# Kernel optimization log

Hardware: AMD Instinct MI355X
Metric: run time of the kernel (lower is better)

The kernel has to match this reference:

```python
import jax, jax.numpy as jnp
import numpy as np
from jax import lax

EPS = 1e-5
DN = ('NCHW', 'OIHW', 'NCHW')


def fastsign(x):
    # forward: sign(x); (STE backward handled in fwdbwd module)
    return jnp.sign(x)


def batchnorm(x, gamma, beta, mean, var):
    # inference-mode BatchNorm2d over channel dim
    inv = gamma / jnp.sqrt(var + EPS)
    return x * inv[None, :, None, None] + (beta - mean * inv)[None, :, None, None]


def avgpool2x2(x):
    B, C, H, W = x.shape
    return x.reshape(B, C, H // 2, 2, W // 2, 2).mean(axis=(3, 5))


def setup_inputs() -> dict:
    key = jax.random.key(0)
    ks = jax.random.split(key, 8)
    inp, B, H, W = 256, 32, 56, 56
    x = jax.random.normal(ks[0], (B, inp, H, W), dtype=jnp.float32)
    w3 = jax.random.normal(ks[1], (inp, inp, 3, 3), dtype=jnp.float32) * 0.05
    g3 = jax.random.uniform(ks[2], (inp,), dtype=jnp.float32, minval=0.5, maxval=1.5)
    b3 = jax.random.normal(ks[3], (inp,), dtype=jnp.float32) * 0.1
    m3 = jax.random.normal(ks[4], (inp,), dtype=jnp.float32) * 0.1
    v3 = jax.random.uniform(ks[5], (inp,), dtype=jnp.float32, minval=0.5, maxval=1.5)
    w1 = jax.random.normal(ks[6], (2 * inp, inp, 1, 1), dtype=jnp.float32) * 0.05
    k2 = jax.random.split(ks[7], 4)
    g1 = jax.random.uniform(k2[0], (2 * inp,), dtype=jnp.float32, minval=0.5, maxval=1.5)
    b1 = jax.random.normal(k2[1], (2 * inp,), dtype=jnp.float32) * 0.1
    m1 = jax.random.normal(k2[2], (2 * inp,), dtype=jnp.float32) * 0.1
    v1 = jax.random.uniform(k2[3], (2 * inp,), dtype=jnp.float32, minval=0.5, maxval=1.5)
    return {"x": x, "w3": w3, "g3": g3, "b3": b3, "m3": m3, "v3": v3,
            "w1": w1, "g1": g1, "b1": b1, "m1": m1, "v1": v1}


def reference(x, w3, g3, b3, m3, v3, w1, g1, b1, m1, v1):
    stride = 2
    # --- conv3x3 branch: binarize act + binarize weight, stride-2 3x3 conv, BN ---
    y = lax.conv_general_dilated(fastsign(x), fastsign(w3),
                                 window_strides=(stride, stride),
                                 padding=((1, 1), (1, 1)),
                                 dimension_numbers=DN)
    y = batchnorm(y, g3, b3, m3, v3)
    # shortcut1: AvgPool2d(2,2) when stride==2
    h = y + avgpool2x2(x)
    # --- pointwise branch: 1x1 binary conv doubling channels, BN ---
    z = lax.conv_general_dilated(fastsign(h), fastsign(w1),
                                 window_strides=(1, 1),
                                 padding=((0, 0), (0, 0)),
                                 dimension_numbers=DN)
    z = batchnorm(z, g1, b1, m1, v1)
    # shortcut2: duplicate channels
    return z + jnp.concatenate((h, h), axis=1)
```

## Files before the change

kernel.cpp:

```cpp
#include <hip/hip_runtime.h>
#include <stdint.h>

#define BB   32
#define CC1  256
#define HH   56
#define WW   56
#define PH   57
#define OHH  28
#define OWW  28
#define NPIX (OHH*OWW)
#define CC2  512
#define EPSV 1e-5f

static __device__ __forceinline__ int popc64(uint64_t v) {
    return __builtin_popcountll(v);
}

__global__ __launch_bounds__(256) void k_binx(const float* __restrict__ x,
                                              uint64_t* __restrict__ xbp,
                                              uint64_t* __restrict__ hbits) {
    int gid = blockIdx.x * 256 + threadIdx.x;
    if (gid < 7296) {
        int b = gid / 228, r = gid % 228;
        xbp[((size_t)(b * PH) * PH + (r >> 2)) * 4 + (r & 3)] = 0ull;
    } else if (gid < 14464) {
        int i = gid - 7296;
        int b = i / 224, r = i % 224;
        xbp[((size_t)(b * PH + (r >> 2) + 1) * PH) * 4 + (r & 3)] = 0ull;
    } else if (gid < 114816) {
        hbits[gid - 14464] = 0ull;
    }

    const int NP = BB * HH * WW;
    int pix = gid % NP;
    int cg  = gid / NP;
    int w = pix % WW;
    int h = (pix / WW) % HH;
    int b = pix / (HH * WW);
    const float* xp = x + ((size_t)(b * CC1 + cg * 64)) * (HH * WW) + h * WW + w;
    uint64_t bits = 0;
    #pragma unroll 8
    for (int c = 0; c < 64; ++c) {
        bits |= (uint64_t)(xp[(size_t)c * (HH * WW)] >= 0.0f) << c;
    }
    xbp[((size_t)((b * PH + h + 1) * PH) + w + 1) * 4 + cg] = bits;
}

__global__ __launch_bounds__(256) void k_packw3(const float* __restrict__ w3,
                                                uint64_t* __restrict__ w3t) {
    int id = blockIdx.x * 256 + threadIdx.x;
    int k   = id % 4;
    int tap = (id / 4) % 9;
    int oc  = id / 36;
    const float* wp = w3 + (size_t)oc * 2304 + (size_t)(k * 64) * 9 + tap;
    uint64_t bits = 0;
    #pragma unroll 8
    for (int c = 0; c < 64; ++c) {
        bits |= (uint64_t)(wp[c * 9] >= 0.0f) << c;
    }
    w3t[((size_t)tap * CC1 + oc) * 4 + k] = bits;
}

__global__ __launch_bounds__(256) void k_prep2(const float* __restrict__ w1,
                                               uint64_t* __restrict__ w1b,
                                               const uint64_t* __restrict__ w3t,
                                               const float* __restrict__ g3,
                                               const float* __restrict__ b3,
                                               const float* __restrict__ m3,
                                               const float* __restrict__ v3,
                                               const float* __restrict__ g1,
                                               const float* __restrict__ b1,
                                               const float* __restrict__ m1,
                                               const float* __restrict__ v1,
                                               float* __restrict__ sc3,
                                               float* __restrict__ bi3,
                                               float* __restrict__ sc1,
                                               float* __restrict__ bi1,
                                               int* __restrict__ ctop,
                                               int* __restrict__ cleft,
                                               int* __restrict__ ccorn) {
    int id = blockIdx.x * 256 + threadIdx.x;
    int k  = id % 4;
    int oc = id / 4;
    const float* wp = w1 + (size_t)oc * 256 + k * 64;
    uint64_t bits = 0;
    #pragma unroll 8
    for (int c = 0; c < 64; ++c) {
        bits |= (uint64_t)(wp[c] >= 0.0f) << c;
    }
    w1b[(size_t)oc * 4 + k] = bits;
    if (k == 0) {
        float s1 = g1[oc] / sqrtf(v1[oc] + EPSV);
        sc1[oc] = s1;
        bi1[oc] = b1[oc] - m1[oc] * s1;
        if (oc < CC1) {
            float s3 = g3[oc] / sqrtf(v3[oc] + EPSV);
            sc3[oc] = s3;
            bi3[oc] = b3[oc] - m3[oc] * s3;
        }
    }
    if (id < CC1) {
        int pt[9];
        #pragma unroll
        for (int t = 0; t < 9; ++t) {
            const uint64_t* p = w3t + ((size_t)t * CC1 + id) * 4;
            pt[t] = popc64(p[0]) + popc64(p[1]) + popc64(p[2]) + popc64(p[3]);
        }
        ctop[id]  = (256 - 2 * pt[0]) + (256 - 2 * pt[1]) + (256 - 2 * pt[2]);
        cleft[id] = (256 - 2 * pt[0]) + (256 - 2 * pt[3]) + (256 - 2 * pt[6]);
        ccorn[id] = (256 - 2 * pt[0]);
    }
}

__global__ __launch_bounds__(256, 4) void k_conv3(const float* __restrict__ x,
                                                  const uint64_t* __restrict__ xbp,
                                                  const uint64_t* __restrict__ w3t,
                                                  const float* __restrict__ sc3,
                                                  const float* __restrict__ bi3,
                                                  const int* __restrict__ ctop,
                                                  const int* __restrict__ cleft,
                                                  const int* __restrict__ ccorn,
                                                  float* __restrict__ hbuf,
                                                  uint64_t* __restrict__ hbits) {
    int loc = blockIdx.x * 256 + threadIdx.x;
    int ow = loc % OWW;
    int oh = (loc / OWW) % OHH;
    int b  = loc / NPIX;
    int ocg = blockIdx.y;

    int tot[8] = {0, 0, 0, 0, 0, 0, 0, 0};
    for (int kh = 0; kh < 3; ++kh) {
        const uint64_t* rp = xbp + ((size_t)((b * PH + 2 * oh + kh) * PH) + 2 * ow) * 4;
        uint64_t t0[4], t1[4], t2[4];
        #pragma unroll
        for (int k = 0; k < 4; ++k) { t0[k] = rp[k]; t1[k] = rp[4 + k]; t2[k] = rp[8 + k]; }
        const uint64_t* wrow = w3t + ((size_t)(kh * 3) * CC1 + ocg * 8) * 4;
        #pragma unroll
        for (int o = 0; o < 8; ++o) {
            const uint64_t* w0  = wrow + (size_t)o * 4;
            const uint64_t* w1p = w0 + (size_t)CC1 * 4;
            const uint64_t* w2p = w0 + (size_t)CC1 * 8;
            int s = tot[o];
            #pragma unroll
            for (int k = 0; k < 4; ++k) s += popc64(t0[k] ^ w0[k]);
            #pragma unroll
            for (int k = 0; k < 4; ++k) s += popc64(t1[k] ^ w1p[k]);
            #pragma unroll
            for (int k = 0; k < 4; ++k) s += popc64(t2[k] ^ w2p[k]);
            tot[o] = s;
        }
    }

    bool top  = (oh == 0);
    bool left = (ow == 0);
    uint64_t hb = 0;
    #pragma unroll
    for (int o = 0; o < 8; ++o) {
        int oc = ocg * 8 + o;
        int corr = (top ? ctop[oc] : 0) + (left ? cleft[oc] : 0)
                 - ((top && left) ? ccorn[oc] : 0);
        float y = (float)(2304 - 2 * tot[o] - corr);
        const float* px = x + ((size_t)(b * CC1 + oc)) * (HH * WW) + (2 * oh) * WW + 2 * ow;
        float2 r0 = *(const float2*)(px);
        float2 r1 = *(const float2*)(px + WW);
        float pool = 0.25f * (r0.x + r0.y + r1.x + r1.y);
        float hv = y * sc3[oc] + bi3[oc] + pool;
        hbuf[((size_t)(b * CC1 + oc)) * NPIX + oh * OWW + ow] = hv;
        hb |= (uint64_t)(hv >= 0.0f) << ((ocg & 7) * 8 + o);
    }
    atomicOr((unsigned long long*)&hbits[(size_t)loc * 4 + (ocg >> 3)],
             (unsigned long long)hb);
}

__global__ __launch_bounds__(256, 4) void k_conv1(const uint64_t* __restrict__ hbits,
                                                  const uint64_t* __restrict__ w1b,
                                                  const float* __restrict__ hbuf,
                                                  const float* __restrict__ sc1,
                                                  const float* __restrict__ bi1,
                                                  float* __restrict__ out) {
    int loc = blockIdx.x * 256 + threadIdx.x;
    int p = loc % NPIX;
    int b = loc / NPIX;
    int ocg = blockIdx.y;

    uint64_t hw[4];
    const uint64_t* hp = hbits + (size_t)loc * 4;
    #pragma unroll
    for (int k = 0; k < 4; ++k) hw[k] = hp[k];

    #pragma unroll
    for (int o = 0; o < 8; ++o) {
        int oc  = ocg * 8 + o;
        int oc2 = oc + CC1;
        const uint64_t* wa = w1b + (size_t)oc  * 4;
        const uint64_t* wb = w1b + (size_t)oc2 * 4;
        int pa = 0, pb = 0;
        #pragma unroll
        for (int k = 0; k < 4; ++k) pa += popc64(hw[k] ^ wa[k]);
        #pragma unroll
        for (int k = 0; k < 4; ++k) pb += popc64(hw[k] ^ wb[k]);
        float hc = hbuf[((size_t)(b * CC1 + oc)) * NPIX + p];
        float za = (float)(256 - 2 * pa) * sc1[oc]  + bi1[oc]  + hc;
        float zb = (float)(256 - 2 * pb) * sc1[oc2] + bi1[oc2] + hc;
        out[((size_t)(b * CC2 + oc))  * NPIX + p] = za;
        out[((size_t)(b * CC2 + oc2)) * NPIX + p] = zb;
    }
}

extern "C" void kernel_launch(void* const* d_in, const int* in_sizes, int n_in,
                              void* d_out, int out_size, void* d_ws, size_t ws_size,
                              hipStream_t stream) {
    const float* x  = (const float*)d_in[0];
    const float* w3 = (const float*)d_in[1];
    const float* g3 = (const float*)d_in[2];
    const float* b3 = (const float*)d_in[3];
    const float* m3 = (const float*)d_in[4];
    const float* v3 = (const float*)d_in[5];
    const float* w1 = (const float*)d_in[6];
    const float* g1 = (const float*)d_in[7];
    const float* b1 = (const float*)d_in[8];
    const float* m1 = (const float*)d_in[9];
    const float* v1 = (const float*)d_in[10];
    float* out = (float*)d_out;

    uint8_t* ws = (uint8_t*)d_ws;
    size_t off = 0;
    uint64_t* xbp   = (uint64_t*)(ws + off); off += (size_t)BB * PH * PH * 4 * 8;
    uint64_t* hbits = (uint64_t*)(ws + off); off += (size_t)BB * NPIX * 4 * 8;
    uint64_t* w3t   = (uint64_t*)(ws + off); off += (size_t)9 * CC1 * 4 * 8;
    uint64_t* w1b   = (uint64_t*)(ws + off); off += (size_t)CC2 * 4 * 8;
    float* sc3 = (float*)(ws + off); off += CC1 * 4;
    float* bi3 = (float*)(ws + off); off += CC1 * 4;
    float* sc1 = (float*)(ws + off); off += CC2 * 4;
    float* bi1 = (float*)(ws + off); off += CC2 * 4;
    int* ctop  = (int*)(ws + off); off += CC1 * 4;
    int* cleft = (int*)(ws + off); off += CC1 * 4;
    int* ccorn = (int*)(ws + off); off += CC1 * 4;
    float* hbuf = (float*)(ws + off);

    k_binx  <<<dim3(401408 / 256), 256, 0, stream>>>(x, xbp, hbits);
    k_packw3<<<dim3(9216 / 256),   256, 0, stream>>>(w3, w3t);
    k_prep2 <<<dim3(2048 / 256),   256, 0, stream>>>(w1, w1b, w3t, g3, b3, m3, v3,
                                                     g1, b1, m1, v1, sc3, bi3, sc1, bi1,
                                                     ctop, cleft, ccorn);
    k_conv3 <<<dim3(98, 32), 256, 0, stream>>>(x, xbp, w3t, sc3, bi3, ctop, cleft, ccorn,
                                               hbuf, hbits);
    k_conv1 <<<dim3(98, 32), 256, 0, stream>>>(hbits, w1b, hbuf, sc1, bi1, out);
}
```

Before: 87.32 us.

## Fuse avgpool into binarize pass and store pool/h intermediates as bf16

The binarize kernel now processes each 2x2 input window per thread. It emits the four sign bit-words and a bf16 pooled average, stored channel-grouped in blocks of 8. The conv3 kernel then reads one 16-byte pooled vector per thread instead of re-reading x from global memory for the shortcut, and writes h as bf16. The conv1 kernel reads that bf16 h. This removes a second full pass over x and halves intermediate traffic, at the cost of bf16 rounding error in the residual terms and possible sign flips of h near zero.

After: 90.09 us. 1.03x slower.

```diff
diff --git a/kernel.cpp b/kernel.cpp
--- a/kernel.cpp
+++ b/kernel.cpp
@@ -12,14 +12,26 @@
 #define CC2  512
 #define EPSV 1e-5f
 
+typedef unsigned short ushortx8 __attribute__((ext_vector_type(8)));
+
 static __device__ __forceinline__ int popc64(uint64_t v) {
     return __builtin_popcountll(v);
 }
-
-__global__ __launch_bounds__(256) void k_binx(const float* __restrict__ x,
-                                              uint64_t* __restrict__ xbp,
-                                              uint64_t* __restrict__ hbits) {
+static __device__ __forceinline__ unsigned short f2bf(float f) {
+    uint32_t u = __float_as_uint(f);
+    u += 0x7FFFu + ((u >> 16) & 1u);
+    return (unsigned short)(u >> 16);
+}
+static __device__ __forceinline__ float bf2f(unsigned short u) {
+    return __uint_as_float(((uint32_t)u) << 16);
+}
+
+__global__ __launch_bounds__(256) void k_binpool(const float* __restrict__ x,
+                                                 uint64_t* __restrict__ xbp,
+                                                 uint64_t* __restrict__ hbits,
+                                                 unsigned short* __restrict__ pool) {
     int gid = blockIdx.x * 256 + threadIdx.x;
+    hbits[gid] = 0ull;
     if (gid < 7296) {
         int b = gid / 228, r = gid % 228;
         xbp[((size_t)(b * PH) * PH + (r >> 2)) * 4 + (r & 3)] = 0ull;
@@ -27,23 +39,39 @@
         int i = gid - 7296;
         int b = i / 224, r = i % 224;
         xbp[((size_t)(b * PH + (r >> 2) + 1) * PH) * 4 + (r & 3)] = 0ull;
-    } else if (gid < 114816) {
-        hbits[gid - 14464] = 0ull;
-    }
-
-    const int NP = BB * HH * WW;
-    int pix = gid % NP;
-    int cg  = gid / NP;
-    int w = pix % WW;
-    int h = (pix / WW) % HH;
-    int b = pix / (HH * WW);
-    const float* xp = x + ((size_t)(b * CC1 + cg * 64)) * (HH * WW) + h * WW + w;
-    uint64_t bits = 0;
-    #pragma unroll 8
-    for (int c = 0; c < 64; ++c) {
-        bits |= (uint64_t)(xp[(size_t)c * (HH * WW)] >= 0.0f) << c;
-    }
-    xbp[((size_t)((b * PH + h + 1) * PH) + w + 1) * 4 + cg] = bits;
+    }
+
+    int cell = gid % NPIX;
+    int cg   = (gid / NPIX) & 3;
+    int b    = gid / (NPIX * 4);
+    int pw = cell % OWW;
+    int ph = cell / OWW;
+    int h0 = 2 * ph, w0 = 2 * pw;
+    const float* base = x + ((size_t)(b * CC1 + cg * 64)) * (HH * WW) + h0 * WW + w0;
+
+    uint64_t s00 = 0, s01 = 0, s10 = 0, s11 = 0;
+    for (int j = 0; j < 8; ++j) {
+        ushortx8 pv;
+        #pragma unroll
+        for (int i = 0; i < 8; ++i) {
+            int c = j * 8 + i;
+            const float* cp = base + (size_t)c * (HH * WW);
+            float2 a = *(const float2*)(cp);
+            float2 d = *(const float2*)(cp + WW);
+            s00 |= (uint64_t)(a.x >= 0.0f) << c;
+            s01 |= (uint64_t)(a.y >= 0.0f) << c;
+            s10 |= (uint64_t)(d.x >= 0.0f) << c;
+            s11 |= (uint64_t)(d.y >= 0.0f) << c;
+            pv[i] = f2bf(0.25f * (a.x + a.y + d.x + d.y));
+        }
+        *(ushortx8*)(pool + ((size_t)((b * 32 + cg * 8 + j) * NPIX + cell)) * 8) = pv;
+    }
+
+    size_t rb = ((size_t)(b * PH + h0 + 1) * PH + w0 + 1) * 4 + cg;
+    xbp[rb]          = s00;
+    xbp[rb + 4]      = s01;
+    xbp[rb + PH * 4]     = s10;
+    xbp[rb + PH * 4 + 4] = s11;
 }
 
 __global__ __launch_bounds__(256) void k_packw3(const float* __restrict__ w3,
@@ -112,19 +140,20 @@
     }
 }
 
-__global__ __launch_bounds__(256, 4) void k_conv3(const float* __restrict__ x,
-                                                  const uint64_t* __restrict__ xbp,
+__global__ __launch_bounds__(256, 4) void k_conv3(const uint64_t* __restrict__ xbp,
                                                   const uint64_t* __restrict__ w3t,
                                                   const float* __restrict__ sc3,
                                                   const float* __restrict__ bi3,
                                                   const int* __restrict__ ctop,
                                                   const int* __restrict__ cleft,
                                                   const int* __restrict__ ccorn,
-                                                  float* __restrict__ hbuf,
+                                                  const unsigned short* __restrict__ pool,
+                                                  unsigned short* __restrict__ hbuf,
                                                   uint64_t* __restrict__ hbits) {
     int loc = blockIdx.x * 256 + threadIdx.x;
-    int ow = loc % OWW;
-    int oh = (loc / OWW) % OHH;
+    int p  = loc % NPIX;
+    int ow = p % OWW;
+    int oh = p / OWW;
     int b  = loc / NPIX;
     int ocg = blockIdx.y;
 
@@ -151,6 +180,8 @@
         }
     }
 
+    ushortx8 pv = *(const ushortx8*)(pool + ((size_t)((b * 32 + ocg) * NPIX + p)) * 8);
+
     bool top  = (oh == 0);
     bool left = (ow == 0);
     uint64_t hb = 0;
@@ -160,12 +191,8 @@
         int corr = (top ? ctop[oc] : 0) + (left ? cleft[oc] : 0)
                  - ((top && left) ? ccorn[oc] : 0);
         float y = (float)(2304 - 2 * tot[o] - corr);
-        const float* px = x + ((size_t)(b * CC1 + oc)) * (HH * WW) + (2 * oh) * WW + 2 * ow;
-        float2 r0 = *(const float2*)(px);
-        float2 r1 = *(const float2*)(px + WW);
-        float pool = 0.25f * (r0.x + r0.y + r1.x + r1.y);
-        float hv = y * sc3[oc] + bi3[oc] + pool;
-        hbuf[((size_t)(b * CC1 + oc)) * NPIX + oh * OWW + ow] = hv;
+        float hv = y * sc3[oc] + bi3[oc] + bf2f(pv[o]);
+        hbuf[((size_t)(b * CC1 + oc)) * NPIX + p] = f2bf(hv);
         hb |= (uint64_t)(hv >= 0.0f) << ((ocg & 7) * 8 + o);
     }
     atomicOr((unsigned long long*)&hbits[(size_t)loc * 4 + (ocg >> 3)],
@@ -174,7 +201,7 @@
 
 __global__ __launch_bounds__(256, 4) void k_conv1(const uint64_t* __restrict__ hbits,
                                                   const uint64_t* __restrict__ w1b,
-                                                  const float* __restrict__ hbuf,
+                                                  const unsigned short* __restrict__ hbuf,
                                                   const float* __restrict__ sc1,
                                                   const float* __restrict__ bi1,
                                                   float* __restrict__ out) {
@@ -199,7 +226,7 @@
         for (int k = 0; k < 4; ++k) pa += popc64(hw[k] ^ wa[k]);
         #pragma unroll
         for (int k = 0; k < 4; ++k) pb += popc64(hw[k] ^ wb[k]);
-        float hc = hbuf[((size_t)(b * CC1 + oc)) * NPIX + p];
+        float hc = bf2f(hbuf[((size_t)(b * CC1 + oc)) * NPIX + p]);
         float za = (float)(256 - 2 * pa) * sc1[oc]  + bi1[oc]  + hc;
         float zb = (float)(256 - 2 * pb) * sc1[oc2] + bi1[oc2] + hc;
         out[((size_t)(b * CC2 + oc))  * NPIX + p] = za;
@@ -236,14 +263,15 @@
     int* ctop  = (int*)(ws + off); off += CC1 * 4;
     int* cleft = (int*)(ws + off); off += CC1 * 4;
     int* ccorn = (int*)(ws + off); off += CC1 * 4;
-    float* hbuf = (float*)(ws + off);
-
-    k_binx  <<<dim3(401408 / 256), 256, 0, stream>>>(x, xbp, hbits);
-    k_packw3<<<dim3(9216 / 256),   256, 0, stream>>>(w3, w3t);
-    k_prep2 <<<dim3(2048 / 256),   256, 0, stream>>>(w1, w1b, w3t, g3, b3, m3, v3,
-                                                     g1, b1, m1, v1, sc3, bi3, sc1, bi1,
-                                                     ctop, cleft, ccorn);
-    k_conv3 <<<dim3(98, 32), 256, 0, stream>>>(x, xbp, w3t, sc3, bi3, ctop, cleft, ccorn,
-                                               hbuf, hbits);
-    k_conv1 <<<dim3(98, 32), 256, 0, stream>>>(hbits, w1b, hbuf, sc1, bi1, out);
-}
+    unsigned short* pool   = (unsigned short*)(ws + off); off += (size_t)BB * CC1 * NPIX * 2;
+    unsigned short* hbuf16 = (unsigned short*)(ws + off); off += (size_t)BB * CC1 * NPIX * 2;
+
+    k_binpool<<<dim3(100352 / 256), 256, 0, stream>>>(x, xbp, hbits, pool);
+    k_packw3 <<<dim3(9216 / 256),   256, 0, stream>>>(w3, w3t);
+    k_prep2  <<<dim3(2048 / 256),   256, 0, stream>>>(w1, w1b, w3t, g3, b3, m3, v3,
+                                                      g1, b1, m1, v1, sc3, bi3, sc1, bi1,
+                                                      ctop, cleft, ccorn);
+    k_conv3  <<<dim3(98, 32), 256, 0, stream>>>(xbp, w3t, sc3, bi3, ctop, cleft, ccorn,
+                                                pool, hbuf16, hbits);
+    k_conv1  <<<dim3(98, 32), 256, 0, stream>>>(hbits, w1b, hbuf16, sc1, bi1, out);
+}
```

## Compute two output pixels per thread, store h in bf16, replace atomics with byte stores

Applied to the files above, without the earlier changes.

Both conv kernels now have each thread handle two adjacent output pixels. Overlapping input bit-planes are loaded once and each weight word serves both pixels, with vectorized float2/ushort2 loads and stores. The fp32 intermediate h buffer becomes bf16 to halve its traffic, but the bf16 rounding changes the residual added to the output and adds precision error. The hbits zeroing pass and the atomicOr are replaced by direct per-byte stores into the packed sign bits, removing atomics, and the grid is halved.

Measured after the change: 90.47 us. +3.6%, slower.

```diff
diff --git a/kernel.cpp b/kernel.cpp
--- a/kernel.cpp
+++ b/kernel.cpp
@@ -9,16 +9,24 @@
 #define OHH  28
 #define OWW  28
 #define NPIX (OHH*OWW)
+#define NPAIR (NPIX/2)
 #define CC2  512
 #define EPSV 1e-5f
 
 static __device__ __forceinline__ int popc64(uint64_t v) {
     return __builtin_popcountll(v);
 }
+static __device__ __forceinline__ unsigned short f2bf(float f) {
+    uint32_t u = __float_as_uint(f);
+    u += 0x7FFFu + ((u >> 16) & 1u);
+    return (unsigned short)(u >> 16);
+}
+static __device__ __forceinline__ float bf2f(unsigned short u) {
+    return __uint_as_float(((uint32_t)u) << 16);
+}
 
 __global__ __launch_bounds__(256) void k_binx(const float* __restrict__ x,
-                                              uint64_t* __restrict__ xbp,
-                                              uint64_t* __restrict__ hbits) {
+                                              uint64_t* __restrict__ xbp) {
     int gid = blockIdx.x * 256 + threadIdx.x;
     if (gid < 7296) {
         int b = gid / 228, r = gid % 228;
@@ -27,8 +35,6 @@
         int i = gid - 7296;
         int b = i / 224, r = i % 224;
         xbp[((size_t)(b * PH + (r >> 2) + 1) * PH) * 4 + (r & 3)] = 0ull;
-    } else if (gid < 114816) {
-        hbits[gid - 14464] = 0ull;
     }
 
     const int NP = BB * HH * WW;
@@ -120,73 +126,99 @@
                                                   const int* __restrict__ ctop,
                                                   const int* __restrict__ cleft,
                                                   const int* __restrict__ ccorn,
-                                                  float* __restrict__ hbuf,
-                                                  uint64_t* __restrict__ hbits) {
-    int loc = blockIdx.x * 256 + threadIdx.x;
-    int ow = loc % OWW;
-    int oh = (loc / OWW) % OHH;
-    int b  = loc / NPIX;
+                                                  unsigned short* __restrict__ hbuf,
+                                                  uint8_t* __restrict__ hbits8) {
+    int t  = blockIdx.x * 256 + threadIdx.x;
+    int pp = t % NPAIR;
+    int b  = t / NPAIR;
+    int p0 = pp * 2;
+    int ow = p0 % OWW;
+    int oh = p0 / OWW;
     int ocg = blockIdx.y;
 
-    int tot[8] = {0, 0, 0, 0, 0, 0, 0, 0};
+    int s0[8] = {0,0,0,0,0,0,0,0};
+    int s1[8] = {0,0,0,0,0,0,0,0};
     for (int kh = 0; kh < 3; ++kh) {
         const uint64_t* rp = xbp + ((size_t)((b * PH + 2 * oh + kh) * PH) + 2 * ow) * 4;
-        uint64_t t0[4], t1[4], t2[4];
-        #pragma unroll
-        for (int k = 0; k < 4; ++k) { t0[k] = rp[k]; t1[k] = rp[4 + k]; t2[k] = rp[8 + k]; }
+        uint64_t tw[20];
+        #pragma unroll
+        for (int k = 0; k < 20; ++k) tw[k] = rp[k];
         const uint64_t* wrow = w3t + ((size_t)(kh * 3) * CC1 + ocg * 8) * 4;
         #pragma unroll
         for (int o = 0; o < 8; ++o) {
             const uint64_t* w0  = wrow + (size_t)o * 4;
             const uint64_t* w1p = w0 + (size_t)CC1 * 4;
             const uint64_t* w2p = w0 + (size_t)CC1 * 8;
-            int s = tot[o];
+            int a0 = s0[o], a1 = s1[o];
             #pragma unroll
-            for (int k = 0; k < 4; ++k) s += popc64(t0[k] ^ w0[k]);
+            for (int k = 0; k < 4; ++k) {
+                uint64_t wv = w0[k];
+                a0 += popc64(tw[k] ^ wv);
+                a1 += popc64(tw[8 + k] ^ wv);
+            }
             #pragma unroll
-            for (int k = 0; k < 4; ++k) s += popc64(t1[k] ^ w1p[k]);
+            for (int k = 0; k < 4; ++k) {
+                uint64_t wv = w1p[k];
+                a0 += popc64(tw[4 + k] ^ wv);
+                a1 += popc64(tw[12 + k] ^ wv);
+            }
             #pragma unroll
-            for (int k = 0; k < 4; ++k) s += popc64(t2[k] ^ w2p[k]);
-            tot[o] = s;
+            for (int k = 0; k < 4; ++k) {
+                uint64_t wv = w2p[k];
+                a0 += popc64(tw[8 + k] ^ wv);
+                a1 += popc64(tw[16 + k] ^ wv);
+            }
+            s0[o] = a0; s1[o] = a1;
         }
     }
 
     bool top  = (oh == 0);
     bool left = (ow == 0);
-    uint64_t hb = 0;
+    unsigned int hb0 = 0, hb1 = 0;
     #pragma unroll
     for (int o = 0; o < 8; ++o) {
         int oc = ocg * 8 + o;
-        int corr = (top ? ctop[oc] : 0) + (left ? cleft[oc] : 0)
-                 - ((top && left) ? ccorn[oc] : 0);
-        float y = (float)(2304 - 2 * tot[o] - corr);
+        int ct = top ? ctop[oc] : 0;
+        int corr0 = ct + (left ? cleft[oc] : 0) - ((top && left) ? ccorn[oc] : 0);
+        float y0 = (float)(2304 - 2 * s0[o] - corr0);
+        float y1 = (float)(2304 - 2 * s1[o] - ct);
         const float* px = x + ((size_t)(b * CC1 + oc)) * (HH * WW) + (2 * oh) * WW + 2 * ow;
-        float2 r0 = *(const float2*)(px);
-        float2 r1 = *(const float2*)(px + WW);
-        float pool = 0.25f * (r0.x + r0.y + r1.x + r1.y);
-        float hv = y * sc3[oc] + bi3[oc] + pool;
-        hbuf[((size_t)(b * CC1 + oc)) * NPIX + oh * OWW + ow] = hv;
-        hb |= (uint64_t)(hv >= 0.0f) << ((ocg & 7) * 8 + o);
-    }
-    atomicOr((unsigned long long*)&hbits[(size_t)loc * 4 + (ocg >> 3)],
-             (unsigned long long)hb);
+        float2 a0 = *(const float2*)(px);
+        float2 a1 = *(const float2*)(px + 2);
+        float2 d0 = *(const float2*)(px + WW);
+        float2 d1 = *(const float2*)(px + WW + 2);
+        float pool0 = 0.25f * (a0.x + a0.y + d0.x + d0.y);
+        float pool1 = 0.25f * (a1.x + a1.y + d1.x + d1.y);
+        float sc = sc3[oc], bi = bi3[oc];
+        float hv0 = y0 * sc + bi + pool0;
+        float hv1 = y1 * sc + bi + pool1;
+        ushort2 st; st.x = f2bf(hv0); st.y = f2bf(hv1);
+        *(ushort2*)(hbuf + ((size_t)(b * CC1 + oc)) * NPIX + p0) = st;
+        hb0 |= (unsigned int)(hv0 >= 0.0f) << o;
+        hb1 |= (unsigned int)(hv1 >= 0.0f) << o;
+    }
+    size_t loc0 = (size_t)(b * NPIX + p0);
+    int boff = (ocg >> 3) * 8 + (ocg & 7);
+    hbits8[loc0 * 32 + boff]        = (uint8_t)hb0;
+    hbits8[(loc0 + 1) * 32 + boff]  = (uint8_t)hb1;
 }
 
 __global__ __launch_bounds__(256, 4) void k_conv1(const uint64_t* __restrict__ hbits,
                                                   const uint64_t* __restrict__ w1b,
-                                                  const float* __restrict__ hbuf,
+                                                  const unsigned short* __restrict__ hbuf,
                                                   const float* __restrict__ sc1,
                                                   const float* __restrict__ bi1,
                                                   float* __restrict__ out) {
-    int loc = blockIdx.x * 256 + threadIdx.x;
-    int p = loc % NPIX;
-    int b = loc / NPIX;
+    int t  = blockIdx.x * 256 + threadIdx.x;
+    int pp = t % NPAIR;
+    int b  = t / NPAIR;
+    int p0 = pp * 2;
     int ocg = blockIdx.y;
 
-    uint64_t hw[4];
-    const uint64_t* hp = hbits + (size_t)loc * 4;
+    const uint64_t* hp = hbits + (size_t)(b * NPIX + p0) * 4;
+    uint64_t h0[4], h1[4];
     #pragma unroll
-    for (int k = 0; k < 4; ++k) hw[k] = hp[k];
+    for (int k = 0; k < 4; ++k) { h0[k] = hp[k]; h1[k] = hp[4 + k]; }
 
     #pragma unroll
     for (int o = 0; o < 8; ++o) {
@@ -194,16 +226,29 @@
         int oc2 = oc + CC1;
         const uint64_t* wa = w1b + (size_t)oc  * 4;
         const uint64_t* wb = w1b + (size_t)oc2 * 4;
-        int pa = 0, pb = 0;
-        #pragma unroll
-        for (int k = 0; k < 4; ++k) pa += popc64(hw[k] ^ wa[k]);
-        #pragma unroll
-        for (int k = 0; k < 4; ++k) pb += popc64(hw[k] ^ wb[k]);
-        float hc = hbuf[((size_t)(b * CC1 + oc)) * NPIX + p];
-        float za = (float)(256 - 2 * pa) * sc1[oc]  + bi1[oc]  + hc;
-        float zb = (float)(256 - 2 * pb) * sc1[oc2] + bi1[oc2] + hc;
-        out[((size_t)(b * CC2 + oc))  * NPIX + p] = za;
-        out[((size_t)(b * CC2 + oc2)) * NPIX + p] = zb;
+        int pa0 = 0, pa1 = 0, pb0 = 0, pb1 = 0;
+        #pragma unroll
+        for (int k = 0; k < 4; ++k) {
+            uint64_t wv = wa[k];
+            pa0 += popc64(h0[k] ^ wv);
+            pa1 += popc64(h1[k] ^ wv);
+        }
+        #pragma unroll
+        for (int k = 0; k < 4; ++k) {
+            uint64_t wv = wb[k];
+            pb0 += popc64(h0[k] ^ wv);
+            pb1 += popc64(h1[k] ^ wv);
+        }
+        ushort2 hcv = *(const ushort2*)(hbuf + ((size_t)(b * CC1 + oc)) * NPIX + p0);
+        float hc0 = bf2f(hcv.x), hc1 = bf2f(hcv.y);
+        float sa = sc1[oc], ba = bi1[oc];
+        float sb = sc1[oc2], bb = bi1[oc2];
+        float2 za; za.x = (float)(256 - 2 * pa0) * sa + ba + hc0;
+                   za.y = (float)(256 - 2 * pa1) * sa + ba + hc1;
+        float2 zb; zb.x = (float)(256 - 2 * pb0) * sb + bb + hc0;
+                   zb.y = (float)(256 - 2 * pb1) * sb + bb + hc1;
+        *(float2*)(out + ((size_t)(b * CC2 + oc))  * NPIX + p0) = za;
+        *(float2*)(out + ((size_t)(b * CC2 + oc2)) * NPIX + p0) = zb;
     }
 }
 
@@ -236,14 +281,14 @@
     int* ctop  = (int*)(ws + off); off += CC1 * 4;
     int* cleft = (int*)(ws + off); off += CC1 * 4;
     int* ccorn = (int*)(ws + off); off += CC1 * 4;
-    float* hbuf = (float*)(ws + off);
-
-    k_binx  <<<dim3(401408 / 256), 256, 0, stream>>>(x, xbp, hbits);
+    unsigned short* hbuf16 = (unsigned short*)(ws + off); off += (size_t)BB * CC1 * NPIX * 2;
+
+    k_binx  <<<dim3(401408 / 256), 256, 0, stream>>>(x, xbp);
     k_packw3<<<dim3(9216 / 256),   256, 0, stream>>>(w3, w3t);
     k_prep2 <<<dim3(2048 / 256),   256, 0, stream>>>(w1, w1b, w3t, g3, b3, m3, v3,
                                                      g1, b1, m1, v1, sc3, bi3, sc1, bi1,
                                                      ctop, cleft, ccorn);
-    k_conv3 <<<dim3(98, 32), 256, 0, stream>>>(x, xbp, w3t, sc3, bi3, ctop, cleft, ccorn,
-                                               hbuf, hbits);
-    k_conv1 <<<dim3(98, 32), 256, 0, stream>>>(hbits, w1b, hbuf, sc1, bi1, out);
-}
+    k_conv3 <<<dim3(49, 32), 256, 0, stream>>>(x, xbp, w3t, sc3, bi3, ctop, cleft, ccorn,
+                                               hbuf16, (uint8_t*)hbits);
+    k_conv1 <<<dim3(49, 32), 256, 0, stream>>>(hbits, w1b, hbuf16, sc1, bi1, out);
+}
```

## Merge prep kernels, store h as bf16, replace atomicOr with byte stores

Applied to the files above, without the earlier changes.

Folds the three preprocessing kernels into one launch with block-range dispatch and computes the border-correction popcounts directly from the float weights, so they no longer depend on the packed w3t. The intermediate h buffer is stored as bf16 instead of fp32, halving its write and read traffic. Per-pixel sign bits are written as individual bytes rather than combined with 64-bit atomicOr, which also removes the need to zero hbits beforehand. Storing h in bf16 loses precision in the residual added to the output and may exceed the tolerance.

Result: slower. 118.9 us (+36.1%).

```diff
diff --git a/kernel.cpp b/kernel.cpp
--- a/kernel.cpp
+++ b/kernel.cpp
@@ -15,100 +15,103 @@
 static __device__ __forceinline__ int popc64(uint64_t v) {
     return __builtin_popcountll(v);
 }
-
-__global__ __launch_bounds__(256) void k_binx(const float* __restrict__ x,
-                                              uint64_t* __restrict__ xbp,
-                                              uint64_t* __restrict__ hbits) {
-    int gid = blockIdx.x * 256 + threadIdx.x;
-    if (gid < 7296) {
-        int b = gid / 228, r = gid % 228;
-        xbp[((size_t)(b * PH) * PH + (r >> 2)) * 4 + (r & 3)] = 0ull;
-    } else if (gid < 14464) {
-        int i = gid - 7296;
-        int b = i / 224, r = i % 224;
-        xbp[((size_t)(b * PH + (r >> 2) + 1) * PH) * 4 + (r & 3)] = 0ull;
-    } else if (gid < 114816) {
-        hbits[gid - 14464] = 0ull;
-    }
-
-    const int NP = BB * HH * WW;
-    int pix = gid % NP;
-    int cg  = gid / NP;
-    int w = pix % WW;
-    int h = (pix / WW) % HH;
-    int b = pix / (HH * WW);
-    const float* xp = x + ((size_t)(b * CC1 + cg * 64)) * (HH * WW) + h * WW + w;
-    uint64_t bits = 0;
-    #pragma unroll 8
-    for (int c = 0; c < 64; ++c) {
-        bits |= (uint64_t)(xp[(size_t)c * (HH * WW)] >= 0.0f) << c;
-    }
-    xbp[((size_t)((b * PH + h + 1) * PH) + w + 1) * 4 + cg] = bits;
-}
-
-__global__ __launch_bounds__(256) void k_packw3(const float* __restrict__ w3,
-                                                uint64_t* __restrict__ w3t) {
-    int id = blockIdx.x * 256 + threadIdx.x;
-    int k   = id % 4;
-    int tap = (id / 4) % 9;
-    int oc  = id / 36;
-    const float* wp = w3 + (size_t)oc * 2304 + (size_t)(k * 64) * 9 + tap;
-    uint64_t bits = 0;
-    #pragma unroll 8
-    for (int c = 0; c < 64; ++c) {
-        bits |= (uint64_t)(wp[c * 9] >= 0.0f) << c;
-    }
-    w3t[((size_t)tap * CC1 + oc) * 4 + k] = bits;
-}
-
-__global__ __launch_bounds__(256) void k_prep2(const float* __restrict__ w1,
-                                               uint64_t* __restrict__ w1b,
-                                               const uint64_t* __restrict__ w3t,
-                                               const float* __restrict__ g3,
-                                               const float* __restrict__ b3,
-                                               const float* __restrict__ m3,
-                                               const float* __restrict__ v3,
-                                               const float* __restrict__ g1,
-                                               const float* __restrict__ b1,
-                                               const float* __restrict__ m1,
-                                               const float* __restrict__ v1,
-                                               float* __restrict__ sc3,
-                                               float* __restrict__ bi3,
-                                               float* __restrict__ sc1,
-                                               float* __restrict__ bi1,
-                                               int* __restrict__ ctop,
-                                               int* __restrict__ cleft,
-                                               int* __restrict__ ccorn) {
-    int id = blockIdx.x * 256 + threadIdx.x;
-    int k  = id % 4;
-    int oc = id / 4;
-    const float* wp = w1 + (size_t)oc * 256 + k * 64;
-    uint64_t bits = 0;
-    #pragma unroll 8
-    for (int c = 0; c < 64; ++c) {
-        bits |= (uint64_t)(wp[c] >= 0.0f) << c;
-    }
-    w1b[(size_t)oc * 4 + k] = bits;
-    if (k == 0) {
-        float s1 = g1[oc] / sqrtf(v1[oc] + EPSV);
-        sc1[oc] = s1;
-        bi1[oc] = b1[oc] - m1[oc] * s1;
-        if (oc < CC1) {
-            float s3 = g3[oc] / sqrtf(v3[oc] + EPSV);
-            sc3[oc] = s3;
-            bi3[oc] = b3[oc] - m3[oc] * s3;
-        }
-    }
-    if (id < CC1) {
-        int pt[9];
-        #pragma unroll
-        for (int t = 0; t < 9; ++t) {
-            const uint64_t* p = w3t + ((size_t)t * CC1 + id) * 4;
-            pt[t] = popc64(p[0]) + popc64(p[1]) + popc64(p[2]) + popc64(p[3]);
-        }
-        ctop[id]  = (256 - 2 * pt[0]) + (256 - 2 * pt[1]) + (256 - 2 * pt[2]);
-        cleft[id] = (256 - 2 * pt[0]) + (256 - 2 * pt[3]) + (256 - 2 * pt[6]);
-        ccorn[id] = (256 - 2 * pt[0]);
+static __device__ __forceinline__ unsigned short f2bf(float f) {
+    uint32_t u = __float_as_uint(f);
+    u += 0x7FFFu + ((u >> 16) & 1u);
+    return (unsigned short)(u >> 16);
+}
+static __device__ __forceinline__ float bf2f(unsigned short u) {
+    return __uint_as_float(((uint32_t)u) << 16);
+}
+
+__global__ __launch_bounds__(256) void k_pre(const float* __restrict__ x,
+                                             const float* __restrict__ w3,
+                                             const float* __restrict__ w1,
+                                             const float* __restrict__ g3,
+                                             const float* __restrict__ b3,
+                                             const float* __restrict__ m3,
+                                             const float* __restrict__ v3,
+                                             const float* __restrict__ g1,
+                                             const float* __restrict__ b1,
+                                             const float* __restrict__ m1,
+                                             const float* __restrict__ v1,
+                                             uint64_t* __restrict__ xbp,
+                                             uint64_t* __restrict__ w3t,
+                                             uint64_t* __restrict__ w1b,
+                                             float* __restrict__ sc3,
+                                             float* __restrict__ bi3,
+                                             float* __restrict__ sc1,
+                                             float* __restrict__ bi1,
+                                             int* __restrict__ ptb) {
+    int bx  = blockIdx.x;
+    int tid = threadIdx.x;
+
+    if (bx < 1568) {
+        int gid = bx * 256 + tid;
+        if (gid < 7296) {
+            int b = gid / 228, r = gid % 228;
+            xbp[((size_t)(b * PH) * PH + (r >> 2)) * 4 + (r & 3)] = 0ull;
+        } else if (gid < 14464) {
+            int i = gid - 7296;
+            int b = i / 224, r = i % 224;
+            xbp[((size_t)(b * PH + (r >> 2) + 1) * PH) * 4 + (r & 3)] = 0ull;
+        }
+        const int NP = BB * HH * WW;
+        int pix = gid % NP;
+        int cg  = gid / NP;
+        int w = pix % WW;
+        int h = (pix / WW) % HH;
+        int b = pix / (HH * WW);
+        const float* xp = x + ((size_t)(b * CC1 + cg * 64)) * (HH * WW) + h * WW + w;
+        uint64_t bits = 0;
+        #pragma unroll 8
+        for (int c = 0; c < 64; ++c) {
+            bits |= (uint64_t)(xp[(size_t)c * (HH * WW)] >= 0.0f) << c;
+        }
+        xbp[((size_t)((b * PH + h + 1) * PH) + w + 1) * 4 + cg] = bits;
+    } else if (bx < 1604) {
+        int id = (bx - 1568) * 256 + tid;
+        int k   = id % 4;
+        int tap = (id / 4) % 9;
+        int oc  = id / 36;
+        const float* wp = w3 + (size_t)oc * 2304 + (size_t)(k * 64) * 9 + tap;
+        uint64_t bits = 0;
+        #pragma unroll 8
+        for (int c = 0; c < 64; ++c) {
+            bits |= (uint64_t)(wp[c * 9] >= 0.0f) << c;
+        }
+        w3t[((size_t)tap * CC1 + oc) * 4 + k] = bits;
+    } else if (bx < 1612) {
+        int id = (bx - 1604) * 256 + tid;
+        int k  = id % 4;
+        int oc = id / 4;
+        const float* wp = w1 + (size_t)oc * 256 + k * 64;
+        uint64_t bits = 0;
+        #pragma unroll 8
+        for (int c = 0; c < 64; ++c) {
+            bits |= (uint64_t)(wp[c] >= 0.0f) << c;
+        }
+        w1b[(size_t)oc * 4 + k] = bits;
+        if (k == 0) {
+            float s1 = g1[oc] / sqrtf(v1[oc] + EPSV);
+            sc1[oc] = s1;
+            bi1[oc] = b1[oc] - m1[oc] * s1;
+            if (oc < CC1) {
+                float s3 = g3[oc] / sqrtf(v3[oc] + EPSV);
+                sc3[oc] = s3;
+                bi3[oc] = b3[oc] - m3[oc] * s3;
+            }
+        }
+    } else {
+        static const int taps[5] = {0, 1, 2, 3, 6};
+        int tt = bx - 1612;
+        int t  = taps[tt];
+        int oc = tid;
+        const float* wp = w3 + (size_t)oc * 2304 + t;
+        int s = 0;
+        #pragma unroll 8
+        for (int c = 0; c < 256; ++c) s += (wp[c * 9] >= 0.0f);
+        ptb[tt * 256 + oc] = 256 - 2 * s;
     }
 }
 
@@ -117,18 +120,17 @@
                                                   const uint64_t* __restrict__ w3t,
                                                   const float* __restrict__ sc3,
                                                   const float* __restrict__ bi3,
-                                                  const int* __restrict__ ctop,
-                                                  const int* __restrict__ cleft,
-                                                  const int* __restrict__ ccorn,
-                                                  float* __restrict__ hbuf,
-                                                  uint64_t* __restrict__ hbits) {
+                                                  const int* __restrict__ ptb,
+                                                  unsigned short* __restrict__ hbuf,
+                                                  uint8_t* __restrict__ hbits8) {
     int loc = blockIdx.x * 256 + threadIdx.x;
-    int ow = loc % OWW;
-    int oh = (loc / OWW) % OHH;
+    int p  = loc % NPIX;
+    int ow = p % OWW;
+    int oh = p / OWW;
     int b  = loc / NPIX;
     int ocg = blockIdx.y;
 
-    int tot[8] = {0, 0, 0, 0, 0, 0, 0, 0};
+    int tot[8] = {0,0,0,0,0,0,0,0};
     for (int kh = 0; kh < 3; ++kh) {
         const uint64_t* rp = xbp + ((size_t)((b * PH + 2 * oh + kh) * PH) + 2 * ow) * 4;
         uint64_t t0[4], t1[4], t2[4];
@@ -153,28 +155,29 @@
 
     bool top  = (oh == 0);
     bool left = (ow == 0);
-    uint64_t hb = 0;
+    unsigned int hb = 0;
     #pragma unroll
     for (int o = 0; o < 8; ++o) {
         int oc = ocg * 8 + o;
-        int corr = (top ? ctop[oc] : 0) + (left ? cleft[oc] : 0)
-                 - ((top && left) ? ccorn[oc] : 0);
+        int corr = 0;
+        if (top)  corr += ptb[oc] + ptb[256 + oc] + ptb[512 + oc];
+        if (left) corr += ptb[oc] + ptb[768 + oc] + ptb[1024 + oc];
+        if (top && left) corr -= ptb[oc];
         float y = (float)(2304 - 2 * tot[o] - corr);
         const float* px = x + ((size_t)(b * CC1 + oc)) * (HH * WW) + (2 * oh) * WW + 2 * ow;
         float2 r0 = *(const float2*)(px);
         float2 r1 = *(const float2*)(px + WW);
         float pool = 0.25f * (r0.x + r0.y + r1.x + r1.y);
         float hv = y * sc3[oc] + bi3[oc] + pool;
-        hbuf[((size_t)(b * CC1 + oc)) * NPIX + oh * OWW + ow] = hv;
-        hb |= (uint64_t)(hv >= 0.0f) << ((ocg & 7) * 8 + o);
-    }
-    atomicOr((unsigned long long*)&hbits[(size_t)loc * 4 + (ocg >> 3)],
-             (unsigned long long)hb);
+        hbuf[((size_t)(b * CC1 + oc)) * NPIX + p] = f2bf(hv);
+        hb |= (unsigned int)(hv >= 0.0f) << o;
+    }
+    hbits8[(size_t)loc * 32 + (ocg >> 3) * 8 + (ocg & 7)] = (uint8_t)hb;
 }
 
 __global__ __launch_bounds__(256, 4) void k_conv1(const uint64_t* __restrict__ hbits,
                                                   const uint64_t* __restrict__ w1b,
-                                                  const float* __restrict__ hbuf,
+                                                  const unsigned short* __restrict__ hbuf,
                                                   const float* __restrict__ sc1,
                                                   const float* __restrict__ bi1,
                                                   float* __restrict__ out) {
@@ -199,7 +202,7 @@
         for (int k = 0; k < 4; ++k) pa += popc64(hw[k] ^ wa[k]);
         #pragma unroll
         for (int k = 0; k < 4; ++k) pb += popc64(hw[k] ^ wb[k]);
-        float hc = hbuf[((size_t)(b * CC1 + oc)) * NPIX + p];
+        float hc = bf2f(hbuf[((size_t)(b * CC1 + oc)) * NPIX + p]);
         float za = (float)(256 - 2 * pa) * sc1[oc]  + bi1[oc]  + hc;
         float zb = (float)(256 - 2 * pb) * sc1[oc2] + bi1[oc2] + hc;
         out[((size_t)(b * CC2 + oc))  * NPIX + p] = za;
@@ -233,17 +236,12 @@
     float* bi3 = (float*)(ws + off); off += CC1 * 4;
     float* sc1 = (float*)(ws + off); off += CC2 * 4;
     float* bi1 = (float*)(ws + off); off += CC2 * 4;
-    int* ctop  = (int*)(ws + off); off += CC1 * 4;
-    int* cleft = (int*)(ws + off); off += CC1 * 4;
-    int* ccorn = (int*)(ws + off); off += CC1 * 4;
-    float* hbuf = (float*)(ws + off);
-
-    k_binx  <<<dim3(401408 / 256), 256, 0, stream>>>(x, xbp, hbits);
-    k_packw3<<<dim3(9216 / 256),   256, 0, stream>>>(w3, w3t);
-    k_prep2 <<<dim3(2048 / 256),   256, 0, stream>>>(w1, w1b, w3t, g3, b3, m3, v3,
-                                                     g1, b1, m1, v1, sc3, bi3, sc1, bi1,
-                                                     ctop, cleft, ccorn);
-    k_conv3 <<<dim3(98, 32), 256, 0, stream>>>(x, xbp, w3t, sc3, bi3, ctop, cleft, ccorn,
-                                               hbuf, hbits);
-    k_conv1 <<<dim3(98, 32), 256, 0, stream>>>(hbits, w1b, hbuf, sc1, bi1, out);
-}
+    int* ptb   = (int*)(ws + off);   off += 5 * CC1 * 4;
+    unsigned short* hbuf16 = (unsigned short*)(ws + off); off += (size_t)BB * CC1 * NPIX * 2;
+
+    k_pre  <<<dim3(1617), 256, 0, stream>>>(x, w3, w1, g3, b3, m3, v3, g1, b1, m1, v1,
+                                            xbp, w3t, w1b, sc3, bi3, sc1, bi1, ptb);
+    k_conv3<<<dim3(98, 32), 256, 0, stream>>>(x, xbp, w3t, sc3, bi3, ptb,
+                                              hbuf16, (uint8_t*)hbits);
+    k_conv1<<<dim3(98, 32), 256, 0, stream>>>(hbits, w1b, hbuf16, sc1, bi1, out);
+}
```
